# Kernel optimization log

Measured on AMD Instinct MI355X. Metric: run time of the kernel, lower is better.

Reference implementation:

```python
import jax, jax.numpy as jnp
import numpy as np

B, T, D_MODEL = 2, 2048, 2048
N_HEAD, N_KV = 16, 4
HEAD_DIM = D_MODEL // N_HEAD  # 128
N_REP = N_HEAD // N_KV        # 4
ROPE_BASE = 10000.0


def setup_inputs() -> dict:
    key = jax.random.key(0)
    ks = jax.random.split(key, 5)
    s = 0.02
    return {
        "x": jax.random.normal(ks[0], (B, T, D_MODEL), dtype=jnp.float32),
        "Wq": jax.random.normal(ks[1], (D_MODEL, N_HEAD * HEAD_DIM), dtype=jnp.float32) * s,
        "Wk": jax.random.normal(ks[2], (D_MODEL, N_KV * HEAD_DIM), dtype=jnp.float32) * s,
        "Wv": jax.random.normal(ks[3], (D_MODEL, N_KV * HEAD_DIM), dtype=jnp.float32) * s,
        "Wo": jax.random.normal(ks[4], (D_MODEL, D_MODEL), dtype=jnp.float32) * s,
    }


def _rope_cos_sin(seq_len, dim, dtype):
    inv_freq = 1.0 / (ROPE_BASE ** (jnp.arange(0, dim, 2, dtype=jnp.float32) / dim))
    t = jnp.arange(seq_len, dtype=jnp.float32)
    freqs = t[:, None] * inv_freq[None, :]          # (T, dim/2)
    emb = jnp.concatenate([freqs, freqs], axis=-1)  # (T, dim)
    return jnp.cos(emb).astype(dtype), jnp.sin(emb).astype(dtype)


def _rotate_half(x):
    half = x.shape[-1] // 2
    return jnp.concatenate([-x[..., half:], x[..., :half]], axis=-1)


def reference(x, Wq, Wk, Wv, Wo):
    Bx, Tx, _ = x.shape
    # projections (weights stored (in, out); equals torch Linear with W^T)
    q = (x @ Wq).reshape(Bx, Tx, N_HEAD, HEAD_DIM).transpose(0, 2, 1, 3)  # (B,H,T,d)
    k = (x @ Wk).reshape(Bx, Tx, N_KV, HEAD_DIM).transpose(0, 2, 1, 3)    # (B,Hkv,T,d)
    v = (x @ Wv).reshape(Bx, Tx, N_KV, HEAD_DIM).transpose(0, 2, 1, 3)

    cos, sin = _rope_cos_sin(Tx, HEAD_DIM, x.dtype)  # (T, d)
    q = q * cos + _rotate_half(q) * sin
    k = k * cos + _rotate_half(k) * sin

    # grouped attention: q grouped by kv head, avoids materializing repeated K/V
    qg = q.reshape(Bx, N_KV, N_REP, Tx, HEAD_DIM)
    scale = 1.0 / np.sqrt(HEAD_DIM)
    att = jnp.einsum('bgrtd,bgsd->bgrts', qg, k) * scale  # (B,Hkv,rep,T,S)
    causal = jnp.tril(jnp.ones((Tx, Tx), dtype=bool))
    att = jnp.where(causal, att, -jnp.inf)
    att = jax.nn.softmax(att, axis=-1)
    y = jnp.einsum('bgrts,bgsd->bgrtd', att, v)           # (B,Hkv,rep,T,d)
    y = y.reshape(Bx, N_HEAD, Tx, HEAD_DIM).transpose(0, 2, 1, 3).reshape(Bx, Tx, D_MODEL)
    return y @ Wo
```

## Files before the change

### kernel.cpp

```cpp
#include <hip/hip_runtime.h>
#include <hip/hip_bf16.h>

typedef unsigned short u16;
typedef unsigned int u32;
typedef __attribute__((ext_vector_type(4))) float f32x4;
typedef __attribute__((ext_vector_type(8))) __bf16 bf16x8;

#define B_   2
#define T_   2048
#define DM   2048
#define NH   16
#define NKV  4
#define HD   128

__device__ __forceinline__ u16 f2bf(float f){
    u32 u = __builtin_bit_cast(u32, f);
    u += 0x7FFFu + ((u >> 16) & 1u);
    return (u16)(u >> 16);
}
__device__ __forceinline__ float bf2f(u16 v){
    return __builtin_bit_cast(float, (u32)v << 16);
}

__device__ __forceinline__ float ex2(float x){
    float r; asm("v_exp_f32 %0, %1" : "=v"(r) : "v"(x)); return r;
}

__device__ __forceinline__ void gld_lds16(const void* g, void* l){
    __builtin_amdgcn_global_load_lds(
        (const __attribute__((address_space(1))) void*)g,
        (__attribute__((address_space(3))) void*)l, 16, 0, 0);
}

__global__ void prep(const float* __restrict__ x,
                     const float* __restrict__ Wq, const float* __restrict__ Wk,
                     const float* __restrict__ Wv, const float* __restrict__ Wo,
                     u16* __restrict__ xb, u16* __restrict__ Wqkv, u16* __restrict__ Wot,
                     float2* __restrict__ tab){
    __shared__ float tile[32][33];
    int bid = blockIdx.x, tid = threadIdx.x;
    if (bid < 8192){
        int i = bid * 256 + tid;
        float4 v = ((const float4*)x)[i];
        ushort4 o;
        o.x = f2bf(v.x); o.y = f2bf(v.y); o.z = f2bf(v.z); o.w = f2bf(v.w);
        ((ushort4*)xb)[i] = o;
    } else if (bid < 18432){
        int tb = bid - 8192;
        int bx = tb % 160, byy = tb / 160;
        const float* W; u16* Out; int N; int nb; int perm;
        if (bx < 64)      { W = Wq; Out = Wqkv;                  N = 2048; nb = bx;      perm = 1; }
        else if (bx < 80) { W = Wk; Out = Wqkv + 2048ull * 2048; N = 512;  nb = bx - 64; perm = 1; }
        else if (bx < 96) { W = Wv; Out = Wqkv + 2560ull * 2048; N = 512;  nb = bx - 80; perm = 0; }
        else              { W = Wo; Out = Wot;                   N = 2048; nb = bx - 96; perm = 0; }
        int n0 = nb * 32, k0 = byy * 32;
        int tx = tid & 31, ty = tid >> 5;
#pragma unroll
        for (int i = 0; i < 4; i++)
            tile[ty + i * 8][tx] = W[(size_t)(k0 + ty + i * 8) * N + n0 + tx];
        __syncthreads();
#pragma unroll
        for (int i = 0; i < 4; i++){
            int n = n0 + ty + i * 8;
            int np = perm ? ((n & ~127) | ((n & 63) << 1) | ((n >> 6) & 1)) : n;
            Out[(size_t)np * 2048 + k0 + tx] = f2bf(tile[tx][ty + i * 8]);
        }
    } else {
        int idx = (bid - 18432) * 256 + tid;
        int i = idx & 63, t = idx >> 6;
        float ang = (float)t * exp2f((float)i * (-13.287712379549449f / 64.0f));
        float sv, cv;
        __sincosf(ang, &sv, &cv);
        tab[idx] = make_float2(cv, sv);
    }
}

#define BARR() asm volatile("s_barrier" ::: "memory")
#define VM0()  asm volatile("s_waitcnt vmcnt(0)" ::: "memory")
#define VM4()  asm volatile("s_waitcnt vmcnt(4)" ::: "memory")
#define VM6()  asm volatile("s_waitcnt vmcnt(6)" ::: "memory")

__global__ __launch_bounds__(512, 2) void gemm192(const u16* __restrict__ A, const u16* __restrict__ Bt,
                                                  u16* __restrict__ Qp, u16* __restrict__ Ktl,
                                                  u16* __restrict__ Vtl, const float2* __restrict__ tab){
    __shared__ __attribute__((aligned(16))) u16 As[2][16384];
    __shared__ __attribute__((aligned(16))) u16 Bs[2][12288];
    const int tid = threadIdx.x;
    const int lane = tid & 63, w = tid >> 6;
    const int wm = w >> 1, wn = w & 1;
    const int tg = lane >> 4, lx = lane & 15;
    int swz = ((int)blockIdx.x & 7) * 32 + ((int)blockIdx.x >> 3);
    const int bx = swz & 15, by = swz >> 4;
    const int m0 = by * 256, n0 = bx * 192;
    const int K = 2048;
    const int kcx = (lane & 7) ^ ((lane >> 3) & 7);

    f32x4 acc[4][6];
    const f32x4 Z = {0.f, 0.f, 0.f, 0.f};
#pragma unroll
    for (int i = 0; i < 4; i++)
#pragma unroll
        for (int j = 0; j < 6; j++) acc[i][j] = Z;
    bf16x8 a_[4][2], b_[2][2];

    auto stA2 = [&](int buf, int h, int kt){
#pragma unroll
        for (int l = 0; l < 2; l++){
            int br = (h * 2 + l) * 64 + w * 8;
            gld_lds16(A + (size_t)(m0 + br + (lane >> 3)) * K + kt * 64 + kcx * 8,
                      &As[buf][br * 64 + lane * 8]);
        }
    };
    auto stB = [&](int buf, int c, int kt){
        int br = (w < 4) ? (c * 32 + w * 8) : (96 + c * 32 + (w - 4) * 8);
        gld_lds16(Bt + (size_t)(n0 + br + (lane >> 3)) * K + kt * 64 + kcx * 8,
                  &Bs[buf][br * 64 + lane * 8]);
    };

#define RA192(BUF) { \
    const char* ab = (const char*)&As[BUF][0]; \
    _Pragma("unroll") for (int mi = 0; mi < 4; mi++){ \
        int rh = wm*64 + mi*16 + lx; \
        _Pragma("unroll") for (int ks = 0; ks < 2; ks++) \
            a_[mi][ks] = *(const bf16x8*)(ab + rh*128 + (((ks*4+tg)*16) ^ ((lx&7)<<4))); \
    } }
#define RB192(BUF, C) { \
    const char* bb = (const char*)&Bs[BUF][0]; \
    _Pragma("unroll") for (int n = 0; n < 2; n++){ \
        int rb = wn*96 + (C)*32 + n*16 + lx; \
        _Pragma("unroll") for (int ks = 0; ks < 2; ks++) \
            b_[n][ks] = *(const bf16x8*)(bb + rb*128 + (((ks*4+tg)*16) ^ ((lx&7)<<4))); \
    } }
#define MM192(C) { \
    __builtin_amdgcn_s_setprio(1); \
    _Pragma("unroll") for (int mi = 0; mi < 4; mi++) \
    _Pragma("unroll") for (int n = 0; n < 2; n++) \
    _Pragma("unroll") for (int ks = 0; ks < 2; ks++) \
        acc[mi][(C)*2+n] = __builtin_amdgcn_mfma_f32_16x16x32_bf16( \
            a_[mi][ks], b_[n][ks], acc[mi][(C)*2+n], 0, 0, 0); \
    __builtin_amdgcn_s_setprio(0); }

    stA2(0, 0, 0); stA2(0, 1, 0); stB(0, 0, 0); stB(0, 1, 0); stB(0, 2, 0);
    stA2(1, 0, 1); stA2(1, 1, 1); stB(1, 0, 1); stB(1, 1, 1);
    VM6(); BARR();

#pragma unroll 1
    for (int it = 0; it < 16; it++){
        const int O  = 2*it + 1;
        const int E2 = (2*it + 2 < 32) ? 2*it + 2 : 31;
        const int O2 = (2*it + 3 < 32) ? 2*it + 3 : 31;
        RA192(0); RB192(0, 0); stB(1, 2, O);
        BARR(); MM192(0); BARR();
        RB192(0, 1); stA2(0, 0, E2); stB(0, 0, E2);
        BARR(); MM192(1); BARR();
        RB192(0, 2); stA2(0, 1, E2); stB(0, 1, E2);
        BARR(); MM192(2); VM6(); BARR();
        RA192(1); RB192(1, 0); stB(0, 2, E2);
        BARR(); MM192(0); BARR();
        RB192(1, 1); stA2(1, 0, O2); stB(1, 0, O2);
        BARR(); MM192(1); BARR();
        RB192(1, 2); stA2(1, 1, O2); stB(1, 1, O2);
        BARR(); MM192(2); VM6(); BARR();
    }

    const float QS = 0.08838834764831845f * 1.4426950408889634f;
#pragma unroll
    for (int mi = 0; mi < 4; mi++){
        int r0 = m0 + wm*64 + mi*16 + tg*4;
#pragma unroll
        for (int ci = 0; ci < 6; ci++){
            int cb = n0 + wn*96 + ci*16;
            int c  = cb + lx;
            if (cb < 2048){
                int ii = (c & 127) >> 1;
#pragma unroll
                for (int j = 0; j < 4; j++){
                    float v = acc[mi][ci][j];
                    float p = __shfl_xor(v, 1);
                    int t = (r0 + j) & 2047;
                    float2 cs = tab[t * 64 + ii];
                    float o = ((lx & 1) ? (v * cs.x + p * cs.y) : (v * cs.x - p * cs.y)) * QS;
                    Qp[(size_t)(r0 + j) * 2048 + c] = f2bf(o);
                }
            } else if (cb < 2560){
                int hk = (c >> 7) & 3;
                int dd = c & 127;
                int ii = dd >> 1;
#pragma unroll
                for (int j = 0; j < 4; j++){
                    int r = r0 + j;
                    int bb2 = r >> 11, tt = r & 2047;
                    float v = acc[mi][ci][j];
                    float p = __shfl_xor(v, 1);
                    float2 cs = tab[tt * 64 + ii];
                    float o = (lx & 1) ? (v * cs.x + p * cs.y) : (v * cs.x - p * cs.y);
                    size_t tb = ((size_t)(bb2 * 4 + hk) * 32 + (tt >> 6)) * 8192;
                    u32 byte = (u32)((tt & 63) * 256) + (((u32)(2 * dd)) ^ ((u32)((tt & 7) << 4)));
                    Ktl[tb + byte / 2] = f2bf(o);
                }
            } else {
                int bb2 = r0 >> 11, ss = r0 & 2047;
                int sb = ss & 63;
                int hk = (c >> 7) & 3;
                int d  = c & 127;
                size_t tb = ((size_t)(bb2 * 4 + hk) * 32 + (ss >> 6)) * 8192;
                u32 swzd = (u32)((d & 7) << 4);
#pragma unroll
                for (int j = 0; j < 4; j++){
                    int s = sb + j;
                    int sig = ((s & 15) << 2) | ((s >> 4) & 3);
                    u32 byte = (u32)(d * 128) + (((u32)(2 * sig)) ^ swzd);
                    Vtl[tb + byte / 2] = f2bf(acc[mi][ci][j]);
                }
            }
        }
    }
}
#undef RA192
#undef RB192
#undef MM192

#define READ_A(QA, BUF) { \
    const char* ab = (const char*)&As[BUF][wm][0]; \
    _Pragma("unroll") for (int i = 0; i < 4; i++){ \
        int rh = ((QA)*4 + i)*16 + lx; \
        _Pragma("unroll") for (int ks = 0; ks < 2; ks++) \
            a_[i][ks] = *(const bf16x8*)(ab + rh*128 + (((ks*4+tg)*16) ^ ((lx&7)<<4))); \
    } }
#define READ_B(QB, BUF) { \
    const char* bb = (const char*)&Bs[BUF][wn>>1][0]; \
    _Pragma("unroll") for (int n = 0; n < 2; n++){ \
        int rbh = (wn&1)*64 + ((QB)*2+n)*16 + lx; \
        _Pragma("unroll") for (int ks = 0; ks < 2; ks++) \
            b_[(QB)*2+n][ks] = *(const bf16x8*)(bb + rbh*128 + (((ks*4+tg)*16) ^ ((lx&7)<<4))); \
    } }
#define MFMA_Q(QA, QB) { \
    __builtin_amdgcn_s_setprio(1); \
    _Pragma("unroll") for (int i = 0; i < 4; i++) \
    _Pragma("unroll") for (int n = 0; n < 2; n++) \
    _Pragma("unroll") for (int ks = 0; ks < 2; ks++) \
        acc[(QA)*4+i][(QB)*2+n] = __builtin_amdgcn_mfma_f32_16x16x32_bf16( \
            a_[i][ks], b_[(QB)*2+n][ks], acc[(QA)*4+i][(QB)*2+n], 0, 0, 0); \
    __builtin_amdgcn_s_setprio(0); }

__global__ __launch_bounds__(512, 2) void gemmWo(const u16* __restrict__ A, const u16* __restrict__ Bt,
                                                 u16* __restrict__ O0){
    __shared__ __attribute__((aligned(16))) u16 As[2][2][8192];
    __shared__ __attribute__((aligned(16))) u16 Bs[2][2][8192];
    const int tid = threadIdx.x;
    const int lane = tid & 63, w = tid >> 6;
    const int wm = w >> 2, wn = w & 3;
    const int tg = lane >> 4, lx = lane & 15;
    int q8 = (int)gridDim.x >> 3;
    int swz = ((int)blockIdx.x & 7) * q8 + ((int)blockIdx.x >> 3);
    int kh = swz >> 7; swz &= 127;
    const int bx = swz & 7, by = swz >> 3;
    const int m0 = by * 256, n0 = bx * 256;
    const int K = 2048;
    const int NIT = 8;
    const int kt0 = kh * 16;
    const int ltMax = 2 * NIT - 1;
    const int kcx = (lane & 7) ^ ((lane >> 3) & 7);

    f32x4 acc[8][4];
    const f32x4 Z = {0.f, 0.f, 0.f, 0.f};
#pragma unroll
    for (int i = 0; i < 8; i++)
#pragma unroll
        for (int j = 0; j < 4; j++) acc[i][j] = Z;
    bf16x8 a_[4][2], b_[4][2];

    auto stA = [&](int buf, int q, int kt){
        int mh = w >> 2;
        int s0 = (w & 3) * 2;
#pragma unroll
        for (int l = 0; l < 2; l++){
            int s = s0 + l;
            gld_lds16(A + (size_t)(m0 + mh*128 + q*64 + s*8 + (lane>>3)) * K + kt*64 + kcx*8,
                      &As[buf][mh][q*4096 + s*512 + lane*8]);
        }
    };
    auto stB = [&](int buf, int q, int kt){
        int bh = w >> 2;
        int hi = (w >> 1) & 1;
        int s0 = (w & 1) * 2;
#pragma unroll
        for (int l = 0; l < 2; l++){
            int s = s0 + l;
            gld_lds16(Bt + (size_t)(n0 + bh*128 + hi*64 + q*32 + s*8 + (lane>>3)) * K + kt*64 + kcx*8,
                      &Bs[buf][bh][hi*4096 + q*2048 + s*512 + lane*8]);
        }
    };

    stA(0, 0, kt0); stB(0, 0, kt0); stA(0, 1, kt0); stB(0, 1, kt0);
    stA(1, 0, kt0 + 1); stB(1, 0, kt0 + 1);
    VM4(); BARR();

#pragma unroll 1
    for (int it = 0; it < NIT; it++){
        const int T1 = kt0 + 2*it + 1;
        const int T2 = kt0 + ((2*it + 2 < ltMax) ? 2*it + 2 : ltMax);
        const int T3 = kt0 + ((2*it + 3 < ltMax) ? 2*it + 3 : ltMax);
        READ_A(0, 0); READ_B(0, 0); stA(1, 1, T1);
        BARR(); MFMA_Q(0, 0); BARR();
        READ_B(1, 0); stB(1, 1, T1);
        BARR(); MFMA_Q(0, 1); BARR();
        READ_A(1, 0); stA(0, 0, T2);
        BARR(); MFMA_Q(1, 0); BARR();
        stB(0, 0, T2);
        BARR(); MFMA_Q(1, 1); VM4(); BARR();
        READ_A(0, 1); READ_B(0, 1); stA(0, 1, T2);
        BARR(); MFMA_Q(0, 0); BARR();
        READ_B(1, 1); stB(0, 1, T2);
        BARR(); MFMA_Q(0, 1); BARR();
        READ_A(1, 1); stA(1, 0, T3);
        BARR(); MFMA_Q(1, 0); BARR();
        stB(1, 0, T3);
        BARR(); MFMA_Q(1, 1); VM4(); BARR();
    }

    u16* C = O0 + (size_t)kh * 4096 * 2048;
#pragma unroll
    for (int mi = 0; mi < 8; mi++)
#pragma unroll
        for (int ni = 0; ni < 4; ni++){
            int r0 = m0 + wm*128 + mi*16 + tg*4;
            int c  = n0 + wn*64 + ni*16 + lx;
#pragma unroll
            for (int j = 0; j < 4; j++)
                C[(size_t)(r0 + j) * 2048 + c] = f2bf(acc[mi][ni][j]);
        }
}

__global__ void reduceWo(const u16* __restrict__ P, float* __restrict__ out){
    size_t t = (size_t)blockIdx.x * 256 + threadIdx.x;
    const u16* p0 = P + t * 8;
    const u16* p1 = P + 4096ull * 2048 + t * 8;
    uint4 a = *(const uint4*)p0;
    uint4 b = *(const uint4*)p1;
    const u16* as = (const u16*)&a;
    const u16* bs = (const u16*)&b;
    float4 o0, o1;
    o0.x = bf2f(as[0]) + bf2f(bs[0]); o0.y = bf2f(as[1]) + bf2f(bs[1]);
    o0.z = bf2f(as[2]) + bf2f(bs[2]); o0.w = bf2f(as[3]) + bf2f(bs[3]);
    o1.x = bf2f(as[4]) + bf2f(bs[4]); o1.y = bf2f(as[5]) + bf2f(bs[5]);
    o1.z = bf2f(as[6]) + bf2f(bs[6]); o1.w = bf2f(as[7]) + bf2f(bs[7]);
    ((float4*)out)[t * 2]     = o0;
    ((float4*)out)[t * 2 + 1] = o1;
}

__global__ __launch_bounds__(256) void attn8(const u16* __restrict__ Q, const u16* __restrict__ Kt,
                                             const u16* __restrict__ Vt, u16* __restrict__ Y){
    __shared__ __attribute__((aligned(16))) u16 Ks[8192];
    __shared__ __attribute__((aligned(16))) u16 Vs[8192];
    __shared__ __attribute__((aligned(16))) u16 Pl[4][1024];
    const int tid = threadIdx.x;
    const int lane = tid & 63, w = tid >> 6;
    const int tg = lane >> 4, lx = lane & 15;
    int gid = blockIdx.x;
    int z = gid & 255, k4 = gid >> 8;
    int j8 = z & 7, h = (z >> 3) & 15, b = z >> 7;
    int qt = (k4 == 0) ? j8 : (k4 == 1) ? 31 - j8 : (k4 == 2) ? j8 + 8 : 23 - j8;
    const int hkv = h >> 2;
    const size_t kvBase = ((size_t)(b * NKV + hkv) * 32) * 8192;
    const f32x4 Z = {0.f, 0.f, 0.f, 0.f};

    auto STAGE_K = [&](int it){
        const u16* kg = Kt + kvBase + (size_t)it * 8192;
#pragma unroll
        for (int i = 0; i < 4; i++){
            int is = w * 4 + i;
            gld_lds16(kg + is * 512 + lane * 8, &Ks[is * 512]);
        }
    };
    auto STAGE_V = [&](int it){
        const u16* vg = Vt + kvBase + (size_t)it * 8192;
#pragma unroll
        for (int i = 0; i < 4; i++){
            int is = w * 4 + i;
            gld_lds16(vg + is * 512 + lane * 8, &Vs[is * 512]);
        }
    };

    const int q0 = qt * 64;
    const int qrow = q0 + w * 16 + lx;
    bf16x8 qfr[4];
#pragma unroll
    for (int kk = 0; kk < 4; kk++)
        qfr[kk] = *(const bf16x8*)(Q + (size_t)(b * T_ + qrow) * DM + h * HD + kk * 32 + tg * 8);
    f32x4 accO[8];
#pragma unroll
    for (int i = 0; i < 8; i++) accO[i] = Z;
    float mr[4] = {-INFINITY, -INFINITY, -INFINITY, -INFINITY};
    float lp[4] = {0.f, 0.f, 0.f, 0.f};
    const int nIter = qt + 1;

    STAGE_K(0); STAGE_V(0);

#pragma unroll 1
    for (int it = 0; it < nIter; it++){
        const bool last = (it + 1 == nIter);
        VM4(); BARR();
        f32x4 sa[4];
#pragma unroll
        for (int c = 0; c < 4; c++) sa[c] = Z;
        __builtin_amdgcn_s_setprio(1);
#pragma unroll
        for (int c = 0; c < 4; c++){
            int s = c * 16 + lx;
            u32 swz = (u32)((s & 7) << 4);
            const char* kb = (const char*)&Ks[0] + s * 256;
#pragma unroll
            for (int kk = 0; kk < 4; kk++){
                bf16x8 kf = *(const bf16x8*)(kb + (((u32)(kk * 64 + tg * 16)) ^ swz));
                sa[c] = __builtin_amdgcn_mfma_f32_16x16x32_bf16(qfr[kk], kf, sa[c], 0, 0, 0);
            }
        }
        __builtin_amdgcn_s_setprio(0);
        BARR();
        if (!last) STAGE_K(it + 1);
        const bool diag = last;
        float tl[4];
#pragma unroll
        for (int j = 0; j < 4; j++){
            float a0 = sa[0][j], a1 = sa[1][j], a2 = sa[2][j], a3 = sa[3][j];
            if (diag){
                int qloc = w * 16 + tg * 4 + j;
                if (lx      > qloc) a0 = -INFINITY;
                if (lx + 16 > qloc) a1 = -INFINITY;
                if (lx + 32 > qloc) a2 = -INFINITY;
                if (lx + 48 > qloc) a3 = -INFINITY;
            }
            sa[0][j] = a0; sa[1][j] = a1; sa[2][j] = a2; sa[3][j] = a3;
            tl[j] = fmaxf(fmaxf(a0, a1), fmaxf(a2, a3));
        }
        int lok = (tl[0] <= mr[0] + 8.f) && (tl[1] <= mr[1] + 8.f) &&
                  (tl[2] <= mr[2] + 8.f) && (tl[3] <= mr[3] + 8.f);
        if (!__all(lok)){
            float corr[4];
#pragma unroll
            for (int j = 0; j < 4; j++){
                float t = tl[j];
                t = fmaxf(t, __shfl_xor(t, 1));
                t = fmaxf(t, __shfl_xor(t, 2));
                t = fmaxf(t, __shfl_xor(t, 4));
                t = fmaxf(t, __shfl_xor(t, 8));
                float mn = fmaxf(mr[j], t);
                corr[j] = ex2(mr[j] - mn);
                mr[j] = mn;
                lp[j] *= corr[j];
            }
#pragma unroll
            for (int dt = 0; dt < 8; dt++){
                f32x4 t = accO[dt];
                t[0] *= corr[0]; t[1] *= corr[1]; t[2] *= corr[2]; t[3] *= corr[3];
                accO[dt] = t;
            }
        }
#pragma unroll
        for (int j = 0; j < 4; j++){
            float mn = mr[j];
            float p0 = ex2(sa[0][j] - mn), p1 = ex2(sa[1][j] - mn);
            float p2 = ex2(sa[2][j] - mn), p3 = ex2(sa[3][j] - mn);
            lp[j] += p0 + p1 + p2 + p3;
            int rr = tg * 4 + j;
            u32 woff = (u32)(rr * 128) + (((u32)(lx * 8)) ^ ((u32)((rr & 7) << 4)));
            u32 r01, r23;
            asm("v_cvt_pk_bf16_f32 %0, %1, %2" : "=v"(r01) : "v"(p0), "v"(p1));
            asm("v_cvt_pk_bf16_f32 %0, %1, %2" : "=v"(r23) : "v"(p2), "v"(p3));
            uint2 pk2 = make_uint2(r01, r23);
            *(uint2*)((char*)&Pl[w][0] + woff) = pk2;
        }
        bf16x8 pf[2];
        {
            char* pb = (char*)&Pl[w][0] + lx * 128;
            u32 swz = (u32)((lx & 7) << 4);
            pf[0] = *(const bf16x8*)(pb + (((u32)(tg * 16))      ^ swz));
            pf[1] = *(const bf16x8*)(pb + (((u32)(tg * 16 + 64)) ^ swz));
        }
        if (last){ VM0(); } else { VM4(); }
        BARR();
        __builtin_amdgcn_s_setprio(1);
#pragma unroll
        for (int dt = 0; dt < 8; dt++){
            int d = dt * 16 + lx;
            u32 swz = (u32)((d & 7) << 4);
            const char* vb = (const char*)&Vs[0] + d * 128;
            bf16x8 vf0 = *(const bf16x8*)(vb + (((u32)(tg * 16))      ^ swz));
            bf16x8 vf1 = *(const bf16x8*)(vb + (((u32)(tg * 16 + 64)) ^ swz));
            accO[dt] = __builtin_amdgcn_mfma_f32_16x16x32_bf16(pf[0], vf0, accO[dt], 0, 0, 0);
            accO[dt] = __builtin_amdgcn_mfma_f32_16x16x32_bf16(pf[1], vf1, accO[dt], 0, 0, 0);
        }
        __builtin_amdgcn_s_setprio(0);
        BARR();
        if (!last) STAGE_V(it + 1);
    }
    float inv[4];
#pragma unroll
    for (int j = 0; j < 4; j++){
        float s = lp[j];
        s += __shfl_xor(s, 1);
        s += __shfl_xor(s, 2);
        s += __shfl_xor(s, 4);
        s += __shfl_xor(s, 8);
        inv[j] = 1.0f / s;
    }
#pragma unroll
    for (int dt = 0; dt < 8; dt++)
#pragma unroll
        for (int j = 0; j < 4; j++){
            int qr = q0 + w * 16 + tg * 4 + j;
            int d = dt * 16 + lx;
            Y[(size_t)(b * T_ + qr) * DM + h * HD + d] = f2bf(accO[dt][j] * inv[j]);
        }
}

extern "C" void kernel_launch(void* const* d_in, const int* in_sizes, int n_in,
                              void* d_out, int out_size, void* d_ws, size_t ws_size,
                              hipStream_t stream){
    const float* x  = (const float*)d_in[0];
    const float* Wq = (const float*)d_in[1];
    const float* Wk = (const float*)d_in[2];
    const float* Wv = (const float*)d_in[3];
    const float* Wo = (const float*)d_in[4];

    char* ws = (char*)d_ws;
    size_t off = 0;
    auto alloc = [&](size_t bytes){ void* p = ws + off; off += (bytes + 255) & ~255ull; return p; };
    u16*    xb   = (u16*)alloc(4096ull * 2048 * 2);
    u16*    Wqkv = (u16*)alloc(3072ull * 2048 * 2);
    u16*    Wot  = (u16*)alloc(2048ull * 2048 * 2);
    u16*    qbb  = (u16*)alloc(4096ull * 2048 * 2);
    u16*    ktl  = (u16*)alloc(2ull * 4 * 32 * 8192 * 2);
    u16*    vtl  = (u16*)alloc(2ull * 4 * 32 * 8192 * 2);
    u16*    ybb  = (u16*)alloc(4096ull * 2048 * 2);
    u16*    pbb  = (u16*)alloc(2ull * 4096 * 2048 * 2);
    float2* tab  = (float2*)alloc(2048ull * 64 * 8);

    prep<<<18944, 256, 0, stream>>>(x, Wq, Wk, Wv, Wo, xb, Wqkv, Wot, tab);

    gemm192<<<256, 512, 0, stream>>>(xb, Wqkv, qbb, ktl, vtl, tab);

    attn8<<<1024, 256, 0, stream>>>(qbb, ktl, vtl, ybb);

    gemmWo<<<256, 512, 0, stream>>>(ybb, Wot, pbb);
    reduceWo<<<4096, 256, 0, stream>>>(pbb, (float*)d_out);
}
```

Before: 196.0 us.

## Compute transposed scores so P stays in registers, skipping LDS round trip

The QK^T MFMA operands are swapped so each lane holds one query row's scores across keys. After bf16 conversion, the softmax probabilities can then feed the PV MFMA directly as the A operand, so the per-warp LDS buffer for P and its write/read traffic go away. The V tile layout written by the QKV GEMM is permuted to match the new key ordering inside P fragments. Each lane now keeps a single running max and sum, so reductions shrink to two cross-group shuffles, plus lane shuffles to broadcast the correction factors. The risk is a mismatch between the new V slot permutation and the register layout of P.

```diff
diff --git a/kernel.cpp b/kernel.cpp
--- a/kernel.cpp
+++ b/kernel.cpp
@@ -208,8 +208,8 @@
 #pragma unroll
                 for (int j = 0; j < 4; j++){
                     int s = sb + j;
-                    int sig = ((s & 15) << 2) | ((s >> 4) & 3);
-                    u32 byte = (u32)(d * 128) + (((u32)(2 * sig)) ^ swzd);
+                    int slot = (s & 32) | (((s >> 2) & 3) << 3) | (((s >> 4) & 1) << 2) | (s & 3);
+                    u32 byte = (u32)(d * 128) + (((u32)(2 * slot)) ^ swzd);
                     Vtl[tb + byte / 2] = f2bf(acc[mi][ci][j]);
                 }
             }
@@ -349,11 +349,10 @@
     ((float4*)out)[t * 2 + 1] = o1;
 }
 
-__global__ __launch_bounds__(256) void attn8(const u16* __restrict__ Q, const u16* __restrict__ Kt,
+__global__ __launch_bounds__(256) void attn9(const u16* __restrict__ Q, const u16* __restrict__ Kt,
                                              const u16* __restrict__ Vt, u16* __restrict__ Y){
     __shared__ __attribute__((aligned(16))) u16 Ks[8192];
     __shared__ __attribute__((aligned(16))) u16 Vs[8192];
-    __shared__ __attribute__((aligned(16))) u16 Pl[4][1024];
     const int tid = threadIdx.x;
     const int lane = tid & 63, w = tid >> 6;
     const int tg = lane >> 4, lx = lane & 15;
@@ -391,8 +390,8 @@
     f32x4 accO[8];
 #pragma unroll
     for (int i = 0; i < 8; i++) accO[i] = Z;
-    float mr[4] = {-INFINITY, -INFINITY, -INFINITY, -INFINITY};
-    float lp[4] = {0.f, 0.f, 0.f, 0.f};
+    float mr = -INFINITY;
+    float lp = 0.f;
     const int nIter = qt + 1;
 
     STAGE_K(0); STAGE_V(0);
@@ -413,70 +412,68 @@
 #pragma unroll
             for (int kk = 0; kk < 4; kk++){
                 bf16x8 kf = *(const bf16x8*)(kb + (((u32)(kk * 64 + tg * 16)) ^ swz));
-                sa[c] = __builtin_amdgcn_mfma_f32_16x16x32_bf16(qfr[kk], kf, sa[c], 0, 0, 0);
+                sa[c] = __builtin_amdgcn_mfma_f32_16x16x32_bf16(kf, qfr[kk], sa[c], 0, 0, 0);
             }
         }
         __builtin_amdgcn_s_setprio(0);
         BARR();
         if (!last) STAGE_K(it + 1);
-        const bool diag = last;
-        float tl[4];
-#pragma unroll
-        for (int j = 0; j < 4; j++){
-            float a0 = sa[0][j], a1 = sa[1][j], a2 = sa[2][j], a3 = sa[3][j];
-            if (diag){
-                int qloc = w * 16 + tg * 4 + j;
-                if (lx      > qloc) a0 = -INFINITY;
-                if (lx + 16 > qloc) a1 = -INFINITY;
-                if (lx + 32 > qloc) a2 = -INFINITY;
-                if (lx + 48 > qloc) a3 = -INFINITY;
+        const int sBase = it * 64 + tg * 4;
+        float tl = -INFINITY;
+#pragma unroll
+        for (int c = 0; c < 4; c++){
+#pragma unroll
+            for (int j = 0; j < 4; j++){
+                float a = sa[c][j];
+                if (last){
+                    if (sBase + c * 16 + j > qrow) a = -INFINITY;
+                }
+                sa[c][j] = a;
+                tl = fmaxf(tl, a);
             }
-            sa[0][j] = a0; sa[1][j] = a1; sa[2][j] = a2; sa[3][j] = a3;
-            tl[j] = fmaxf(fmaxf(a0, a1), fmaxf(a2, a3));
-        }
-        int lok = (tl[0] <= mr[0] + 8.f) && (tl[1] <= mr[1] + 8.f) &&
-                  (tl[2] <= mr[2] + 8.f) && (tl[3] <= mr[3] + 8.f);
-        if (!__all(lok)){
-            float corr[4];
+        }
+        if (!__all(tl <= mr + 8.f)){
+            float t = fmaxf(tl, __shfl_xor(tl, 16));
+            t = fmaxf(t, __shfl_xor(t, 32));
+            float mn = fmaxf(mr, t);
+            float corrq = ex2(mr - mn);
+            mr = mn;
+            lp *= corrq;
+            float corrO[4];
+#pragma unroll
+            for (int j = 0; j < 4; j++)
+                corrO[j] = __shfl(corrq, (lane & 48) + ((lane >> 4) << 2) + j);
+#pragma unroll
+            for (int dt = 0; dt < 8; dt++){
+                f32x4 t2 = accO[dt];
+                t2[0] *= corrO[0]; t2[1] *= corrO[1]; t2[2] *= corrO[2]; t2[3] *= corrO[3];
+                accO[dt] = t2;
+            }
+        }
+        float p[4][4];
+#pragma unroll
+        for (int c = 0; c < 4; c++)
 #pragma unroll
             for (int j = 0; j < 4; j++){
-                float t = tl[j];
-                t = fmaxf(t, __shfl_xor(t, 1));
-                t = fmaxf(t, __shfl_xor(t, 2));
-                t = fmaxf(t, __shfl_xor(t, 4));
-                t = fmaxf(t, __shfl_xor(t, 8));
-                float mn = fmaxf(mr[j], t);
-                corr[j] = ex2(mr[j] - mn);
-                mr[j] = mn;
-                lp[j] *= corr[j];
+                float v = ex2(sa[c][j] - mr);
+                p[c][j] = v;
+                lp += v;
             }
-#pragma unroll
-            for (int dt = 0; dt < 8; dt++){
-                f32x4 t = accO[dt];
-                t[0] *= corr[0]; t[1] *= corr[1]; t[2] *= corr[2]; t[3] *= corr[3];
-                accO[dt] = t;
-            }
-        }
-#pragma unroll
-        for (int j = 0; j < 4; j++){
-            float mn = mr[j];
-            float p0 = ex2(sa[0][j] - mn), p1 = ex2(sa[1][j] - mn);
-            float p2 = ex2(sa[2][j] - mn), p3 = ex2(sa[3][j] - mn);
-            lp[j] += p0 + p1 + p2 + p3;
-            int rr = tg * 4 + j;
-            u32 woff = (u32)(rr * 128) + (((u32)(lx * 8)) ^ ((u32)((rr & 7) << 4)));
-            u32 r01, r23;
-            asm("v_cvt_pk_bf16_f32 %0, %1, %2" : "=v"(r01) : "v"(p0), "v"(p1));
-            asm("v_cvt_pk_bf16_f32 %0, %1, %2" : "=v"(r23) : "v"(p2), "v"(p3));
-            uint2 pk2 = make_uint2(r01, r23);
-            *(uint2*)((char*)&Pl[w][0] + woff) = pk2;
-        }
-        bf16x8 pf[2];
+        bf16x8 pa0, pa1;
         {
-            char* pb = (char*)&Pl[w][0] + lx * 128;
-            u32 swz = (u32)((lx & 7) << 4);
-            pf[0] = *(const bf16x8*)(pb + (((u32)(tg * 16))      ^ swz));
-            pf[1] = *(const bf16x8*)(pb + (((u32)(tg * 16 + 64)) ^ swz));
+            u32 w0, w1, w2, w3;
+            asm("v_cvt_pk_bf16_f32 %0, %1, %2" : "=v"(w0) : "v"(p[0][0]), "v"(p[0][1]));
+            asm("v_cvt_pk_bf16_f32 %0, %1, %2" : "=v"(w1) : "v"(p[0][2]), "v"(p[0][3]));
+            asm("v_cvt_pk_bf16_f32 %0, %1, %2" : "=v"(w2) : "v"(p[1][0]), "v"(p[1][1]));
+            asm("v_cvt_pk_bf16_f32 %0, %1, %2" : "=v"(w3) : "v"(p[1][2]), "v"(p[1][3]));
+            u32 r[4] = {w0, w1, w2, w3};
+            pa0 = __builtin_bit_cast(bf16x8, *(uint4*)r);
+            asm("v_cvt_pk_bf16_f32 %0, %1, %2" : "=v"(w0) : "v"(p[2][0]), "v"(p[2][1]));
+            asm("v_cvt_pk_bf16_f32 %0, %1, %2" : "=v"(w1) : "v"(p[2][2]), "v"(p[2][3]));
+            asm("v_cvt_pk_bf16_f32 %0, %1, %2" : "=v"(w2) : "v"(p[3][0]), "v"(p[3][1]));
+            asm("v_cvt_pk_bf16_f32 %0, %1, %2" : "=v"(w3) : "v"(p[3][2]), "v"(p[3][3]));
+            u32 r2[4] = {w0, w1, w2, w3};
+            pa1 = __builtin_bit_cast(bf16x8, *(uint4*)r2);
         }
         if (last){ VM0(); } else { VM4(); }
         BARR();
@@ -488,23 +485,20 @@
             const char* vb = (const char*)&Vs[0] + d * 128;
             bf16x8 vf0 = *(const bf16x8*)(vb + (((u32)(tg * 16))      ^ swz));
             bf16x8 vf1 = *(const bf16x8*)(vb + (((u32)(tg * 16 + 64)) ^ swz));
-            accO[dt] = __builtin_amdgcn_mfma_f32_16x16x32_bf16(pf[0], vf0, accO[dt], 0, 0, 0);
-            accO[dt] = __builtin_amdgcn_mfma_f32_16x16x32_bf16(pf[1], vf1, accO[dt], 0, 0, 0);
+            accO[dt] = __builtin_amdgcn_mfma_f32_16x16x32_bf16(pa0, vf0, accO[dt], 0, 0, 0);
+            accO[dt] = __builtin_amdgcn_mfma_f32_16x16x32_bf16(pa1, vf1, accO[dt], 0, 0, 0);
         }
         __builtin_amdgcn_s_setprio(0);
         BARR();
         if (!last) STAGE_V(it + 1);
     }
+    lp += __shfl_xor(lp, 16);
+    lp += __shfl_xor(lp, 32);
+    float invq = 1.0f / lp;
     float inv[4];
 #pragma unroll
-    for (int j = 0; j < 4; j++){
-        float s = lp[j];
-        s += __shfl_xor(s, 1);
-        s += __shfl_xor(s, 2);
-        s += __shfl_xor(s, 4);
-        s += __shfl_xor(s, 8);
-        inv[j] = 1.0f / s;
-    }
+    for (int j = 0; j < 4; j++)
+        inv[j] = __shfl(invq, (lane & 48) + ((lane >> 4) << 2) + j);
 #pragma unroll
     for (int dt = 0; dt < 8; dt++)
 #pragma unroll
@@ -541,7 +535,7 @@
 
     gemm192<<<256, 512, 0, stream>>>(xb, Wqkv, qbb, ktl, vtl, tab);
 
-    attn8<<<1024, 256, 0, stream>>>(qbb, ktl, vtl, ybb);
+    attn9<<<1024, 256, 0, stream>>>(qbb, ktl, vtl, ybb);
 
     gemmWo<<<256, 512, 0, stream>>>(ybb, Wot, pbb);
     reduceWo<<<4096, 256, 0, stream>>>(pbb, (float*)d_out);
```

Result: faster. 186.9 us (-4.7%).
